# Optimization experiments

Hardware: AMD Instinct MI355X
Metric: run time of the kernel (lower is better)

Reference implementation:

```python
import jax, jax.numpy as jnp
import numpy as np

BETA_2 = 1.0
LAMBDA_2 = 1.0


def _segment_logsumexp(x, seg, num_segments):
    # numerically stable segment logsumexp; empty segments -> 0.0
    m = jax.ops.segment_max(x, seg, num_segments=num_segments)
    m_safe = jnp.where(jnp.isfinite(m), m, 0.0)
    s = jax.ops.segment_sum(jnp.exp(x - m_safe[seg]), seg, num_segments=num_segments)
    lse = m_safe + jnp.log(s)
    return jnp.where(s > 0, lse, 0.0)


def setup_inputs() -> dict:
    key = jax.random.key(0)
    k1, k2, k3, k4, k5 = jax.random.split(key, 5)
    num_nodes, d, num_edges, num_graphs = 100000, 64, 3200000, 256
    Q2 = jax.random.normal(k1, (num_nodes, d), dtype=jnp.float32)
    K2 = jax.random.normal(k2, (num_nodes, d), dtype=jnp.float32)
    c_2 = jax.random.randint(k3, (num_edges,), 0, num_nodes)
    u_2 = jax.random.randint(k4, (num_edges,), 0, num_nodes)
    batch = jnp.sort(jax.random.randint(k5, (num_nodes,), 0, num_graphs))
    return {"Q2": Q2, "K2": K2, "c_2": c_2, "u_2": u_2, "batch": batch,
            "num_graphs": num_graphs}


def reference(Q2, K2, c_2, u_2, batch, num_graphs):
    num_nodes, d = Q2.shape
    scale = d ** 0.5
    # pairwise dot over edges: [E]
    ell_2 = jnp.sum(Q2[c_2] * K2[u_2], axis=-1) / scale
    # segment logsumexp grouped by destination node c: [N]
    lse_2 = _segment_logsumexp(BETA_2 * ell_2, c_2, num_nodes)
    # scatter-add per-node lse into per-graph energy: [G]
    graph_lse = jax.ops.segment_sum(lse_2, batch, num_segments=num_graphs)
    E = (LAMBDA_2 / BETA_2) * graph_lse
    return E
```

## Files before the change

kernel.cpp:

```cpp
#include <hip/hip_runtime.h>
#include <hip/hip_fp8.h>
#include <math.h>

typedef __attribute__((ext_vector_type(2))) float fv2;

#if defined(__has_builtin)
#  if __has_builtin(__builtin_amdgcn_cvt_pk_f32_fp8) && \
      __has_builtin(__builtin_amdgcn_cvt_pk_fp8_f32)
#    define PE_HAVE_FP8_BUILTINS 1
#  endif
#endif

#define MAX_NB 1024
#define NPB 256
#define NPB_SHIFT 8
#define B2_EPT 16
#define B2_CHUNK (B2_EPT * 256)
#define CPB 8
#define RT 1024

__device__ __forceinline__ unsigned pack4_fp8(float a, float b, float c, float d) {
#ifdef PE_HAVE_FP8_BUILTINS
    int w = 0;
    w = __builtin_amdgcn_cvt_pk_fp8_f32(a, b, w, false);
    w = __builtin_amdgcn_cvt_pk_fp8_f32(c, d, w, true);
    return (unsigned)w;
#else
    unsigned r = 0;
    r |= (unsigned)__hip_fp8_e4m3(a).__x;
    r |= (unsigned)__hip_fp8_e4m3(b).__x << 8;
    r |= (unsigned)__hip_fp8_e4m3(c).__x << 16;
    r |= (unsigned)__hip_fp8_e4m3(d).__x << 24;
    return r;
#endif
}

__device__ __forceinline__ float dot4w_fp8(unsigned qa, unsigned ka, float acc) {
#ifdef PE_HAVE_FP8_BUILTINS
    fv2 q0 = __builtin_amdgcn_cvt_pk_f32_fp8((int)qa, false);
    fv2 q1 = __builtin_amdgcn_cvt_pk_f32_fp8((int)qa, true);
    fv2 k0 = __builtin_amdgcn_cvt_pk_f32_fp8((int)ka, false);
    fv2 k1 = __builtin_amdgcn_cvt_pk_f32_fp8((int)ka, true);
    acc = fmaf(q0.x, k0.x, acc);
    acc = fmaf(q0.y, k0.y, acc);
    acc = fmaf(q1.x, k1.x, acc);
    acc = fmaf(q1.y, k1.y, acc);
    return acc;
#else
#pragma unroll
    for (int j = 0; j < 4; ++j) {
        __hip_fp8_e4m3 qv, kv;
        qv.__x = (qa >> (8 * j)) & 0xff;
        kv.__x = (ka >> (8 * j)) & 0xff;
        acc = fmaf((float)qv, (float)kv, acc);
    }
    return acc;
#endif
}

__device__ __forceinline__ float dot16_fp8(const uint4& q, const uint4& k) {
    float d = 0.0f;
    d = dot4w_fp8(q.x, k.x, d);
    d = dot4w_fp8(q.y, k.y, d);
    d = dot4w_fp8(q.z, k.z, d);
    d = dot4w_fp8(q.w, k.w, d);
    return d;
}

__device__ __forceinline__ float red4(float d) {
    d += __shfl_xor(d, 1, 64);
    d += __shfl_xor(d, 2, 64);
    return d;
}

__global__ __launch_bounds__(256) void pe_convert_kernel(
    const float* __restrict__ Q,
    const float* __restrict__ K,
    unsigned* __restrict__ Qq,
    unsigned* __restrict__ Kq,
    float* __restrict__ node_sum,
    float* __restrict__ out,
    int n4,
    int num_nodes,
    int num_graphs) {
    const int i = blockIdx.x * blockDim.x + threadIdx.x;
    if (i < num_nodes) node_sum[i] = 0.0f;
    if (i < num_graphs) out[i] = 0.0f;
    if (i >= n4) return;

    const float4 q = ((const float4*)Q)[i];
    const float4 k = ((const float4*)K)[i];
    Qq[i] = pack4_fp8(q.x, q.y, q.z, q.w);
    Kq[i] = pack4_fp8(k.x, k.y, k.z, k.w);
}

__global__ __launch_bounds__(256) void pe_count_kernel(
    const int* __restrict__ c,
    unsigned* __restrict__ cnt_mat,
    int num_edges, int nb, int nblk) {
    __shared__ unsigned h[MAX_NB];
    const int tid = threadIdx.x;
    const int blk = blockIdx.x;
    for (int b = tid; b < nb; b += 256) h[b] = 0u;
    __syncthreads();

    const int estart = blk * B2_CHUNK;
    const int ecount = min(B2_CHUNK, num_edges - estart);
    const int n4 = ecount >> 2;
    const int4* c4 = (const int4*)(c + estart);
    for (int k = tid; k < n4; k += 256) {
        const int4 v = c4[k];
        atomicAdd(&h[v.x >> NPB_SHIFT], 1u);
        atomicAdd(&h[v.y >> NPB_SHIFT], 1u);
        atomicAdd(&h[v.z >> NPB_SHIFT], 1u);
        atomicAdd(&h[v.w >> NPB_SHIFT], 1u);
    }
    for (int e = (n4 << 2) + tid; e < ecount; e += 256)
        atomicAdd(&h[c[estart + e] >> NPB_SHIFT], 1u);
    __syncthreads();

    for (int b = tid; b < nb; b += 256)
        cnt_mat[(size_t)b * nblk + blk] = h[b];
}

__global__ __launch_bounds__(256) void pe_matscan_kernel(
    unsigned* __restrict__ cnt_mat,
    unsigned* __restrict__ bucket_cnt,
    int nblk) {
    __shared__ unsigned s[256];
    const int t = threadIdx.x;
    unsigned* row = cnt_mat + (size_t)blockIdx.x * nblk;
    unsigned carry = 0u;
    for (int t0 = 0; t0 < nblk; t0 += 256) {
        const int i = t0 + t;
        const unsigned v = (i < nblk) ? row[i] : 0u;
        s[t] = v;
        __syncthreads();
        for (int off = 1; off < 256; off <<= 1) {
            const unsigned mine = s[t];
            const unsigned add = (t >= off) ? s[t - off] : 0u;
            __syncthreads();
            s[t] = mine + add;
            __syncthreads();
        }
        if (i < nblk) row[i] = carry + (s[t] - v);
        carry += s[255];
        __syncthreads();
    }
    if (t == 0) bucket_cnt[blockIdx.x] = carry;
}

__global__ __launch_bounds__(1024) void pe_scan_kernel(
    const unsigned* __restrict__ bucket_cnt,
    unsigned* __restrict__ bucket_base,
    int nb) {
    __shared__ unsigned s[MAX_NB];
    const int t = threadIdx.x;
    const unsigned v = (t < nb) ? bucket_cnt[t] : 0u;
    s[t] = v;
    __syncthreads();
    for (int off = 1; off < MAX_NB; off <<= 1) {
        const unsigned mine = s[t];
        const unsigned add = (t >= off) ? s[t - off] : 0u;
        __syncthreads();
        s[t] = mine + add;
        __syncthreads();
    }
    if (t < nb) bucket_base[t] = s[t] - v;
    if (t == 0) bucket_base[nb] = s[MAX_NB - 1];
}

__global__ __launch_bounds__(256) void pe_binify_kernel(
    const int* __restrict__ c,
    const int* __restrict__ u,
    const unsigned* __restrict__ cnt_mat,
    const unsigned* __restrict__ bucket_base,
    unsigned* __restrict__ recs,
    int num_edges, int nb, int nblk) {
    __shared__ unsigned rank[MAX_NB];
    __shared__ unsigned basesh[MAX_NB];

    const int tid = threadIdx.x;
    const int blk = blockIdx.x;
    const int estart = blk * B2_CHUNK;
    const int ecount = min(B2_CHUNK, num_edges - estart);

    for (int b = tid; b < nb; b += 256) {
        rank[b] = 0u;
        basesh[b] = bucket_base[b] + cnt_mat[(size_t)b * nblk + blk];
    }
    __syncthreads();

    unsigned rw[B2_EPT];
    int rb[B2_EPT];
    unsigned rr[B2_EPT];

    if (ecount == B2_CHUNK) {
        const int4* c4 = (const int4*)(c + estart);
        const int4* u4 = (const int4*)(u + estart);
#pragma unroll
        for (int jj = 0; jj < 4; ++jj) {
            const int k = jj * 256 + tid;
            const int4 cv = c4[k];
            const int4 uv = u4[k];
            const int j = jj * 4;
            rb[j + 0] = cv.x >> NPB_SHIFT;
            rb[j + 1] = cv.y >> NPB_SHIFT;
            rb[j + 2] = cv.z >> NPB_SHIFT;
            rb[j + 3] = cv.w >> NPB_SHIFT;
            rw[j + 0] = ((unsigned)uv.x << NPB_SHIFT) | (unsigned)(cv.x & (NPB - 1));
            rw[j + 1] = ((unsigned)uv.y << NPB_SHIFT) | (unsigned)(cv.y & (NPB - 1));
            rw[j + 2] = ((unsigned)uv.z << NPB_SHIFT) | (unsigned)(cv.z & (NPB - 1));
            rw[j + 3] = ((unsigned)uv.w << NPB_SHIFT) | (unsigned)(cv.w & (NPB - 1));
            rr[j + 0] = atomicAdd(&rank[rb[j + 0]], 1u);
            rr[j + 1] = atomicAdd(&rank[rb[j + 1]], 1u);
            rr[j + 2] = atomicAdd(&rank[rb[j + 2]], 1u);
            rr[j + 3] = atomicAdd(&rank[rb[j + 3]], 1u);
        }
    } else {
#pragma unroll
        for (int j = 0; j < B2_EPT; ++j) {
            rb[j] = -1;
            const int e = estart + j * 256 + tid;
            if (e < num_edges) {
                const int cc = c[e];
                const int uu = u[e];
                rb[j] = cc >> NPB_SHIFT;
                rw[j] = ((unsigned)uu << NPB_SHIFT) | (unsigned)(cc & (NPB - 1));
                rr[j] = atomicAdd(&rank[rb[j]], 1u);
            }
        }
    }

#pragma unroll
    for (int j = 0; j < B2_EPT; ++j) {
        if (rb[j] >= 0) recs[basesh[rb[j]] + rr[j]] = rw[j];
    }
}

__global__ __launch_bounds__(256) void pe_dotred_kernel(
    const unsigned* __restrict__ Qq,
    const unsigned* __restrict__ Kq,
    const unsigned* __restrict__ recs,
    const unsigned* __restrict__ bucket_base,
    float* __restrict__ node_sum,
    int num_nodes) {
    __shared__ uint4 qlds[NPB * 4];
    __shared__ float acc[NPB];
    __shared__ unsigned rlds[RT];

    const int B = blockIdx.x / CPB;
    const int chunk = blockIdx.x - B * CPB;
    const int t = threadIdx.x;
    const int g = t >> 2;
    const int sub = t & 3;
    const float inv_scale = 0.125f;

    const int nrows = min(NPB, num_nodes - B * NPB);
    const uint4* qsrc = (const uint4*)Qq + (size_t)B * NPB * 4;
    for (int i = t; i < nrows * 4; i += 256) qlds[i] = qsrc[i];
    acc[t] = 0.0f;

    const unsigned s0 = bucket_base[B];
    const unsigned len = bucket_base[B + 1] - s0;
    const unsigned r0 = s0 + (unsigned)(((unsigned long long)len * chunk) / CPB);
    const unsigned r1 = s0 + (unsigned)(((unsigned long long)len * (chunk + 1)) / CPB);

    for (unsigned t0 = r0; t0 < r1; t0 += RT) {
        const unsigned n = min((unsigned)RT, r1 - t0);
        __syncthreads();
        for (unsigned i = t; i < n; i += 256) rlds[i] = recs[t0 + i];
        __syncthreads();
        for (unsigned i = g; i < n; i += 64) {
            const unsigned rec = rlds[i];
            const unsigned uu = rec >> NPB_SHIFT;
            const unsigned local = rec & (NPB - 1);
            const uint4 k = *(const uint4*)(Kq + (size_t)uu * 16 + sub * 4);
            const uint4 q = qlds[local * 4 + sub];
            const float d = red4(dot16_fp8(q, k));
            if (sub == 0) atomicAdd(&acc[local], __expf(d * inv_scale));
        }
    }
    __syncthreads();

    if (t < nrows && acc[t] != 0.0f)
        atomicAdd(&node_sum[B * NPB + t], acc[t]);
}

__global__ __launch_bounds__(256) void pe_node_kernel(
    const float* __restrict__ node_sum,
    const int* __restrict__ batch,
    float* __restrict__ out,
    int num_nodes) {
    const int n = blockIdx.x * blockDim.x + threadIdx.x;
    const bool valid = (n < num_nodes);
    const int nc = valid ? n : (num_nodes - 1);

    const float s = valid ? node_sum[nc] : 0.0f;
    float lse = (s > 0.0f) ? logf(s) : 0.0f;
    if (!valid) lse = 0.0f;
    const int b = batch[nc];

    const int b0 = __shfl(b, 0, 64);
    const bool uniform = __all(b == b0);
    if (uniform) {
        lse += __shfl_xor(lse, 1, 64);
        lse += __shfl_xor(lse, 2, 64);
        lse += __shfl_xor(lse, 4, 64);
        lse += __shfl_xor(lse, 8, 64);
        lse += __shfl_xor(lse, 16, 64);
        lse += __shfl_xor(lse, 32, 64);
        if ((threadIdx.x & 63) == 0 && lse != 0.0f) {
            atomicAdd(&out[b0], lse);
        }
    } else {
        if (valid && lse != 0.0f) {
            atomicAdd(&out[b], lse);
        }
    }
}


__global__ __launch_bounds__(256) void pe_edge_kernel(
    const unsigned* __restrict__ Qq,
    const unsigned* __restrict__ Kq,
    const int* __restrict__ c,
    const int* __restrict__ u,
    float* __restrict__ node_sum,
    int num_edges) {
    const int tid = blockIdx.x * blockDim.x + threadIdx.x;
    const int group = tid >> 2;
    const int sub = tid & 3;
    const int ngroups = (gridDim.x * blockDim.x) >> 2;
    const float inv_scale = 0.125f;

    const int E4 = num_edges & ~3;

    for (int base = group * 4; base < E4; base += ngroups * 4) {
        const int4 ci = *(const int4*)(c + base);
        const int4 ui = *(const int4*)(u + base);

        const uint4 q0 = *(const uint4*)(Qq + (size_t)ci.x * 16 + sub * 4);
        const uint4 q1 = *(const uint4*)(Qq + (size_t)ci.y * 16 + sub * 4);
        const uint4 q2 = *(const uint4*)(Qq + (size_t)ci.z * 16 + sub * 4);
        const uint4 q3 = *(const uint4*)(Qq + (size_t)ci.w * 16 + sub * 4);
        const uint4 k0 = *(const uint4*)(Kq + (size_t)ui.x * 16 + sub * 4);
        const uint4 k1 = *(const uint4*)(Kq + (size_t)ui.y * 16 + sub * 4);
        const uint4 k2 = *(const uint4*)(Kq + (size_t)ui.z * 16 + sub * 4);
        const uint4 k3 = *(const uint4*)(Kq + (size_t)ui.w * 16 + sub * 4);

        float d0 = red4(dot16_fp8(q0, k0));
        float d1 = red4(dot16_fp8(q1, k1));
        float d2 = red4(dot16_fp8(q2, k2));
        float d3 = red4(dot16_fp8(q3, k3));

        const float dsel = (sub == 0) ? d0 : (sub == 1) ? d1 : (sub == 2) ? d2 : d3;
        const int csel = (sub == 0) ? ci.x : (sub == 1) ? ci.y : (sub == 2) ? ci.z : ci.w;
        atomicAdd(&node_sum[csel], __expf(dsel * inv_scale));
    }

    for (int e = E4 + group; e < num_edges; e += ngroups) {
        const int cc = c[e];
        const int uu = u[e];
        const uint4 q = *(const uint4*)(Qq + (size_t)cc * 16 + sub * 4);
        const uint4 k = *(const uint4*)(Kq + (size_t)uu * 16 + sub * 4);
        float d = red4(dot16_fp8(q, k));
        if (sub == 0) atomicAdd(&node_sum[cc], __expf(d * inv_scale));
    }
}

extern "C" void kernel_launch(void* const* d_in, const int* in_sizes, int n_in,
                              void* d_out, int out_size, void* d_ws, size_t ws_size,
                              hipStream_t stream) {
    const float* Q2 = (const float*)d_in[0];
    const float* K2 = (const float*)d_in[1];
    const int* c_2 = (const int*)d_in[2];
    const int* u_2 = (const int*)d_in[3];
    const int* batch = (const int*)d_in[4];

    const int num_nodes = in_sizes[4];
    const int num_edges = in_sizes[2];
    const int num_graphs = out_size;
    const int d = in_sizes[0] / num_nodes;
    const size_t row_elems = (size_t)num_nodes * d;
    const size_t row_bytes = row_elems;

    const int nb = (num_nodes + NPB - 1) >> NPB_SHIFT;
    const int nblk = (num_edges + B2_CHUNK - 1) / B2_CHUNK;

    unsigned* Qq = (unsigned*)d_ws;
    unsigned* Kq = Qq + row_bytes / 4;
    unsigned* meta = Kq + row_bytes / 4;
    unsigned* bucket_cnt = meta;
    unsigned* bucket_base = meta + MAX_NB;
    float* node_sum_b = (float*)(meta + 2 * MAX_NB + 16);
    const size_t ns_pad = ((size_t)num_nodes + 15) & ~(size_t)15;
    unsigned* recs = (unsigned*)node_sum_b + ns_pad;
    unsigned* cnt_mat = recs + num_edges;
    float* node_sum_f = (float*)meta;
    float* out = (float*)d_out;

    const size_t need_binned = row_bytes * 2 + (size_t)(2 * MAX_NB + 16) * 4 +
                               ns_pad * 4 + (size_t)num_edges * 4 +
                               (size_t)nb * nblk * 4;
    const bool use_binned = (nb <= MAX_NB) && (ws_size >= need_binned) &&
                            (d == 64) && (num_nodes <= (1 << 24));

    float* node_sum = use_binned ? node_sum_b : node_sum_f;

    {
        const int n4 = (int)(row_elems / 4);
        const int block = 256;
        const int grid = (n4 + block - 1) / block;
        pe_convert_kernel<<<grid, block, 0, stream>>>(
            Q2, K2, Qq, Kq, node_sum, out, n4, num_nodes, num_graphs);
    }

    if (use_binned) {
        pe_count_kernel<<<nblk, 256, 0, stream>>>(c_2, cnt_mat,
                                                  num_edges, nb, nblk);
        pe_matscan_kernel<<<nb, 256, 0, stream>>>(cnt_mat, bucket_cnt, nblk);
        pe_scan_kernel<<<1, 1024, 0, stream>>>(bucket_cnt, bucket_base, nb);
        pe_binify_kernel<<<nblk, 256, 0, stream>>>(c_2, u_2, cnt_mat,
                                                   bucket_base, recs,
                                                   num_edges, nb, nblk);
        pe_dotred_kernel<<<nb * CPB, 256, 0, stream>>>(Qq, Kq, recs,
                                                       bucket_base,
                                                       node_sum, num_nodes);
    } else {
        pe_edge_kernel<<<8192, 256, 0, stream>>>(Qq, Kq, c_2, u_2,
                                                 node_sum, num_edges);
    }

    {
        const int block = 256;
        const int grid = (num_nodes + block - 1) / block;
        pe_node_kernel<<<grid, block, 0, stream>>>(node_sum, batch, out,
                                                   num_nodes);
    }
}
```

Before: 216.1 us.

## Stage binify scatter through LDS and map dotred blocks to XCDs

The binify kernel now computes a local exclusive scan of per-bucket counts, stages records in shared memory sorted by bucket, and writes them out in order, so the global scatter becomes mostly contiguous runs instead of random 4-byte writes. The dotred kernel remaps block indices so that all chunks of a bucket land on the same XCD, which is meant to improve L2 reuse of the Q tile and K rows. CPB drops from 8 to 4 so there are fewer blocks per bucket. The change adds shared memory (about 28KB more per block in binify), which may lower occupancy, and tightens the node-count limit to 2^23 because the bucket index is stored as an unsigned short.

Measured after the change: 197.8 us. -8.5%, faster.

```diff
diff --git a/kernel.cpp b/kernel.cpp
--- a/kernel.cpp
+++ b/kernel.cpp
@@ -16,8 +16,9 @@
 #define NPB_SHIFT 8
 #define B2_EPT 16
 #define B2_CHUNK (B2_EPT * 256)
-#define CPB 8
+#define CPB 4
 #define RT 1024
+#define NXCD 8
 
 __device__ __forceinline__ unsigned pack4_fp8(float a, float b, float c, float d) {
 #ifdef PE_HAVE_FP8_BUILTINS
@@ -178,17 +179,20 @@
     unsigned* __restrict__ recs,
     int num_edges, int nb, int nblk) {
     __shared__ unsigned rank[MAX_NB];
+    __shared__ unsigned lstart[MAX_NB];
     __shared__ unsigned basesh[MAX_NB];
+    __shared__ unsigned srec[B2_CHUNK];
+    __shared__ unsigned short sbuk[B2_CHUNK];
+    __shared__ unsigned wtot[4];
 
     const int tid = threadIdx.x;
     const int blk = blockIdx.x;
     const int estart = blk * B2_CHUNK;
     const int ecount = min(B2_CHUNK, num_edges - estart);
 
-    for (int b = tid; b < nb; b += 256) {
-        rank[b] = 0u;
+    for (int b = tid; b < MAX_NB; b += 256) rank[b] = 0u;
+    for (int b = tid; b < nb; b += 256)
         basesh[b] = bucket_base[b] + cnt_mat[(size_t)b * nblk + blk];
-    }
     __syncthreads();
 
     unsigned rw[B2_EPT];
@@ -231,10 +235,48 @@
             }
         }
     }
+    __syncthreads();
+
+    {
+        const int b4 = tid * 4;
+        const unsigned v0 = rank[b4 + 0];
+        const unsigned v1 = rank[b4 + 1];
+        const unsigned v2 = rank[b4 + 2];
+        const unsigned v3 = rank[b4 + 3];
+        const unsigned tsum = v0 + v1 + v2 + v3;
+        unsigned incl = tsum;
+        const int lane = tid & 63;
+#pragma unroll
+        for (int off = 1; off < 64; off <<= 1) {
+            const unsigned nv = __shfl_up(incl, off, 64);
+            if (lane >= off) incl += nv;
+        }
+        if (lane == 63) wtot[tid >> 6] = incl;
+        __syncthreads();
+        unsigned woff = 0;
+        const int w = tid >> 6;
+        for (int i = 0; i < w; ++i) woff += wtot[i];
+        const unsigned ebase = woff + incl - tsum;
+        lstart[b4 + 0] = ebase;
+        lstart[b4 + 1] = ebase + v0;
+        lstart[b4 + 2] = ebase + v0 + v1;
+        lstart[b4 + 3] = ebase + v0 + v1 + v2;
+    }
+    __syncthreads();
 
 #pragma unroll
     for (int j = 0; j < B2_EPT; ++j) {
-        if (rb[j] >= 0) recs[basesh[rb[j]] + rr[j]] = rw[j];
+        if (rb[j] >= 0) {
+            const unsigned pos = lstart[rb[j]] + rr[j];
+            srec[pos] = rw[j];
+            sbuk[pos] = (unsigned short)rb[j];
+        }
+    }
+    __syncthreads();
+
+    for (int i = tid; i < ecount; i += 256) {
+        const int b = sbuk[i];
+        recs[basesh[b] + (unsigned)i - lstart[b]] = srec[i];
     }
 }
 
@@ -244,15 +286,20 @@
     const unsigned* __restrict__ recs,
     const unsigned* __restrict__ bucket_base,
     float* __restrict__ node_sum,
-    int num_nodes) {
+    int num_nodes, int nb) {
     __shared__ uint4 qlds[NPB * 4];
     __shared__ float acc[NPB];
     __shared__ unsigned rlds[RT];
 
-    const int B = blockIdx.x / CPB;
-    const int chunk = blockIdx.x - B * CPB;
+    const int g = blockIdx.x;
+    const int xcd = g & (NXCD - 1);
+    const int slot = g >> 3;
+    const int B = xcd + NXCD * (slot / CPB);
+    const int chunk = slot - (slot / CPB) * CPB;
+    if (B >= nb) return;
+
     const int t = threadIdx.x;
-    const int g = t >> 2;
+    const int gteam = t >> 2;
     const int sub = t & 3;
     const float inv_scale = 0.125f;
 
@@ -271,7 +318,7 @@
         __syncthreads();
         for (unsigned i = t; i < n; i += 256) rlds[i] = recs[t0 + i];
         __syncthreads();
-        for (unsigned i = g; i < n; i += 64) {
+        for (unsigned i = gteam; i < n; i += 64) {
             const unsigned rec = rlds[i];
             const unsigned uu = rec >> NPB_SHIFT;
             const unsigned local = rec & (NPB - 1);
@@ -404,7 +451,7 @@
                                ns_pad * 4 + (size_t)num_edges * 4 +
                                (size_t)nb * nblk * 4;
     const bool use_binned = (nb <= MAX_NB) && (ws_size >= need_binned) &&
-                            (d == 64) && (num_nodes <= (1 << 24));
+                            (d == 64) && (num_nodes <= (1 << 23));
 
     float* node_sum = use_binned ? node_sum_b : node_sum_f;
 
@@ -424,9 +471,12 @@
         pe_binify_kernel<<<nblk, 256, 0, stream>>>(c_2, u_2, cnt_mat,
                                                    bucket_base, recs,
                                                    num_edges, nb, nblk);
-        pe_dotred_kernel<<<nb * CPB, 256, 0, stream>>>(Qq, Kq, recs,
+        {
+            const int grid = NXCD * ((nb + NXCD - 1) / NXCD) * CPB;
+            pe_dotred_kernel<<<grid, 256, 0, stream>>>(Qq, Kq, recs,
                                                        bucket_base,
-                                                       node_sum, num_nodes);
+                                                       node_sum, num_nodes, nb);
+        }
     } else {
         pe_edge_kernel<<<8192, 256, 0, stream>>>(Qq, Kq, c_2, u_2,
                                                  node_sum, num_edges);
```
